# Kernel optimization log

Hardware: AMD Instinct MI355X
Metric: run time of the kernel (lower is better)

The kernel has to match this reference:

```python
import jax, jax.numpy as jnp
import numpy as np

B, L, D = 4, 2048, 1024
H, DK, DV = 16, 64, 64
SCALE = float((4 * DK) ** 0.5)
EPS = 1e-6


def setup_inputs() -> dict:
    key = jax.random.key(0)
    ks = jax.random.split(key, 16)
    s_in = 1.0 / np.sqrt(D)
    inp = {}
    for i, name in enumerate(["q_a", "k_a", "v_a", "q_s", "k_s", "v_s"]):
        inp[name] = jax.random.normal(ks[i], (B, L, D), dtype=jnp.float32)
    # weights stored as [in, out] so projection is x @ W (equivalent math to nn.Linear)
    for j, name in enumerate(["Wqa", "Wka", "Wva", "Wqs", "Wks", "Wvs", "Wfc"]):
        inp[name] = jax.random.normal(ks[6 + j], (D, D), dtype=jnp.float32) * s_in
    inp["gamma"] = jnp.ones((D,), dtype=jnp.float32)
    inp["beta"] = jnp.zeros((D,), dtype=jnp.float32)
    return inp


def _proj(x, W, dh):
    # [B,L,D] @ [D, H*dh] -> [B,H,L,dh]
    return (x @ W).reshape(B, -1, H, dh).transpose(0, 2, 1, 3)


def reference(q_a, k_a, v_a, q_s, k_s, v_s, Wqa, Wka, Wva, Wqs, Wks, Wvs, Wfc, gamma, beta):
    residual = q_a + q_s
    qa = _proj(q_a, Wqa, DK)
    ka = _proj(k_a, Wka, DK)
    va = _proj(v_a, Wva, DV)
    qs = _proj(q_s, Wqs, DK)
    ks_ = _proj(k_s, Wks, DK)
    vs = _proj(v_s, Wvs, DV)
    # a2a + a2s + s2a + s2s == (qa+qs) @ (ka+ks)^T  (algebraic identity)
    q = qa + qs
    k = ka + ks_
    v = va + vs
    scores = jnp.einsum("bhqd,bhkd->bhqk", q, k) / SCALE
    attn = jax.nn.softmax(scores, axis=-1)  # dropout = identity (eval)
    out = jnp.einsum("bhqk,bhkd->bhqd", attn, v)  # [B,H,L,DV]
    out = out.transpose(0, 2, 1, 3).reshape(B, L, H * DV)
    out = out @ Wfc + residual
    mu = jnp.mean(out, axis=-1, keepdims=True)
    var = jnp.var(out, axis=-1, keepdims=True)
    out = (out - mu) * jax.lax.rsqrt(var + EPS) * gamma + beta
    return out
```

## Files before the change

kernel.cpp:

```cpp
#include <hip/hip_runtime.h>
#include <hip/hip_bf16.h>
#include <stdint.h>

typedef __attribute__((ext_vector_type(4))) float f32x4;
typedef __attribute__((ext_vector_type(16))) float f32x16;
typedef __attribute__((ext_vector_type(8))) short short8;
typedef __attribute__((ext_vector_type(2))) int int2v;

#define DEV static __device__ __forceinline__

DEV unsigned short f2bf(float f) {
  unsigned u = __float_as_uint(f);
  u += 0x7fffu + ((u >> 16) & 1u);
  return (unsigned short)(u >> 16);
}

DEV uint32_t cvtpk(float a, float b) {
  uint32_t r;
  asm("v_cvt_pk_bf16_f32 %0, %1, %2" : "=v"(r) : "v"(a), "v"(b));
  return r;
}

DEV int2v pl32(int a, int b) {
  return __builtin_amdgcn_permlane32_swap(a, b, false, false);
}

typedef const __attribute__((address_space(1))) void* gas_ptr;
typedef __attribute__((address_space(3))) void* las_ptr;

DEV void gload_lds16(const void* g, void* l) {
  __builtin_amdgcn_global_load_lds((gas_ptr)g, (las_ptr)l, 16, 0, 0);
}

struct CvtArgs {
  const float* in[6];
  unsigned short* out[6];
};

__global__ __launch_bounds__(256) void cvt_kernel(CvtArgs a, int n4) {
  const float* __restrict__ in = a.in[blockIdx.y];
  unsigned short* __restrict__ out = a.out[blockIdx.y];
  int idx = blockIdx.x * blockDim.x + threadIdx.x;
  int stride = gridDim.x * blockDim.x;
  for (int i = idx; i < n4; i += stride) {
    float4 v = reinterpret_cast<const float4*>(in)[i];
    ushort4 o;
    o.x = f2bf(v.x); o.y = f2bf(v.y); o.z = f2bf(v.z); o.w = f2bf(v.w);
    reinterpret_cast<ushort4*>(out)[i] = o;
  }
}

struct TcvtArgs {
  const float* src[7];
  unsigned short* dst[7];
  int stride[7];
  int koff[7];
};

__global__ __launch_bounds__(256) void tcvt_kernel(TcvtArgs a) {
  const int which = blockIdx.z;
  const float* __restrict__ src = a.src[which];
  unsigned short* __restrict__ dst = a.dst[which];
  const int dstStride = a.stride[which], kOff = a.koff[which];
  __shared__ float tile[32][33];
  int tx = threadIdx.x & 31;
  int ty = threadIdx.x >> 5;
  int n0 = blockIdx.x * 32;
  int k0 = blockIdx.y * 32;
#pragma unroll
  for (int i = 0; i < 4; i++)
    tile[ty + 8 * i][tx] = src[(size_t)(k0 + ty + 8 * i) * 1024 + n0 + tx];
  __syncthreads();
#pragma unroll
  for (int i = 0; i < 4; i++) {
    int n = n0 + ty + 8 * i;
    dst[(size_t)n * dstStride + kOff + k0 + tx] = f2bf(tile[tx][ty + 8 * i]);
  }
}

struct G3Args {
  const unsigned short* A1[3];
  const unsigned short* A2[3];
  const unsigned short* WT[3];
  unsigned short* out[3];
};

__global__ __launch_bounds__(512, 2) void gemm3_kernel(G3Args g) {
  __shared__ unsigned short As[2][256 * 64];
  __shared__ unsigned short Bs[2][256 * 64];
  const int orig = blockIdx.x;
  const int swz = (orig & 7) * 48 + (orig >> 3);
  const int which = swz >> 7;
  const int bid = swz & 127;
  const unsigned short* __restrict__ A1 = g.A1[which];
  const unsigned short* __restrict__ A2 = g.A2[which];
  const unsigned short* __restrict__ WT = g.WT[which];
  unsigned short* __restrict__ outp = g.out[which];

  const int tid = threadIdx.x;
  const int lane = tid & 63;
  const int w = tid >> 6;
  const int mt = bid >> 2, nt = bid & 3;
  const int m0 = mt * 256, n0 = nt * 256;
  const int wr = w >> 2, wc = w & 3;

  const int lr = lane >> 3;
  const int lcsw = (((lane & 7) ^ lr) << 3);
  const int aW = (w < 4) ? (w * 8) : (128 + (w - 4) * 8);
  const int bW = w * 8;

  const int la = lane & 15;
  const int szb = (lane & 7) << 4;
  int cF[2];
#pragma unroll
  for (int ks = 0; ks < 2; ks++)
    cF[ks] = (((ks << 6) + ((lane >> 4) << 4)) ^ szb) >> 1;
  const int arA = (wr * 128 + la) * 64;
  const int brB = (wc * 64 + la) * 64;

  f32x4 zero4 = {0.f, 0.f, 0.f, 0.f};
  f32x4 acc[8][4];
#pragma unroll
  for (int mf = 0; mf < 8; mf++)
#pragma unroll
    for (int nf = 0; nf < 4; nf++) acc[mf][nf] = zero4;

  short8 bf[4][2];

  auto STAGE_B = [&](int buf, int kk) {
#pragma unroll
    for (int r = 0; r < 4; r++)
      gload_lds16(WT + (size_t)(n0 + bW + r * 64 + lr) * 2048 + kk + lcsw,
                  &Bs[buf][(bW + r * 64) * 64 + lane * 8]);
  };
  auto STAGE_A = [&](int buf, int kk, int r) {
    const unsigned short* Ab = (kk < 1024) ? A1 : A2;
    const int ka = kk & 1023;
    gload_lds16(Ab + (size_t)(m0 + aW + r * 32 + lr) * 1024 + ka + lcsw,
                &As[buf][(aW + r * 32) * 64 + lane * 8]);
  };

  STAGE_B(0, 0);
#pragma unroll
  for (int r = 0; r < 4; r++) STAGE_A(0, 0, r);
  asm volatile("s_waitcnt vmcnt(3)" ::: "memory");
  __builtin_amdgcn_s_barrier();
  __builtin_amdgcn_sched_barrier(0);

  for (int kt = 0; kt < 32; kt++) {
    const int cur = kt & 1;
    const int nbuf = cur ^ 1;
    const int kk = kt << 6;
    const int nk = (kt < 31) ? (kk + 64) : kk;
#pragma unroll
    for (int p = 0; p < 4; p++) {
      if (p == 0) {
#pragma unroll
        for (int nf = 0; nf < 4; nf++)
#pragma unroll
          for (int ks = 0; ks < 2; ks++)
            bf[nf][ks] = *reinterpret_cast<const short8*>(&Bs[cur][brB + nf * 1024 + cF[ks]]);
      }
      short8 af[2][2];
#pragma unroll
      for (int mi = 0; mi < 2; mi++)
#pragma unroll
        for (int ks = 0; ks < 2; ks++)
          af[mi][ks] =
              *reinterpret_cast<const short8*>(&As[cur][arA + (2 * p + mi) * 1024 + cF[ks]]);
      if (p == 0) STAGE_B(nbuf, nk);
      STAGE_A(nbuf, nk, p);
      asm volatile("s_waitcnt lgkmcnt(0)" ::: "memory");
      __builtin_amdgcn_sched_barrier(0);
      __builtin_amdgcn_s_setprio(1);
#pragma unroll
      for (int mi = 0; mi < 2; mi++)
#pragma unroll
        for (int nf = 0; nf < 4; nf++)
#pragma unroll
          for (int ks = 0; ks < 2; ks++)
            acc[2 * p + mi][nf] = __builtin_amdgcn_mfma_f32_16x16x32_bf16(
                af[mi][ks], bf[nf][ks], acc[2 * p + mi][nf], 0, 0, 0);
      __builtin_amdgcn_s_setprio(0);
      __builtin_amdgcn_sched_barrier(0);
      if (p == 3) asm volatile("s_waitcnt vmcnt(3)" ::: "memory");
      else        asm volatile("s_waitcnt vmcnt(7)" ::: "memory");
      __builtin_amdgcn_s_barrier();
      __builtin_amdgcn_sched_barrier(0);
    }
  }
  asm volatile("s_waitcnt vmcnt(0)" ::: "memory");

#pragma unroll
  for (int mf = 0; mf < 8; mf++) {
#pragma unroll
    for (int nf = 0; nf < 4; nf++) {
      const int col = n0 + wc * 64 + nf * 16 + (lane & 15);
      const int rbase = m0 + wr * 128 + mf * 16 + ((lane >> 4) << 2);
      const int h = col >> 6, d = col & 63;
      if (which < 2) {
#pragma unroll
        for (int r = 0; r < 4; r++) {
          const int m = rbase + r;
          const int b = m >> 11, l = m & 2047;
          outp[((size_t)((b * 16 + h) * 2048 + l)) * 64 + d] = f2bf(acc[mf][nf][r]);
        }
      } else {
        const int m = rbase;
        const int b = m >> 11, l = m & 2047;
        const int bh = b * 16 + h;
        ushort4 o;
        o.x = f2bf(acc[mf][nf][0]);
        o.y = f2bf(acc[mf][nf][1]);
        o.z = f2bf(acc[mf][nf][2]);
        o.w = f2bf(acc[mf][nf][3]);
        *reinterpret_cast<ushort4*>(
            outp + (size_t)(bh * 64 + (l >> 5)) * 2048 + d * 32 + (l & 31)) = o;
      }
    }
  }
}

__global__ __launch_bounds__(256) void gemmfc_kernel(const unsigned short* __restrict__ A1,
                                                     const unsigned short* __restrict__ WT,
                                                     float* __restrict__ outp) {
  __shared__ unsigned short As[128 * 32];
  __shared__ unsigned short Bs[128 * 32];
  const int orig = blockIdx.x;
  const int bid = (orig & 7) * 64 + (orig >> 3);
  const int tid = threadIdx.x;
  const int lane = tid & 63;
  const int w = tid >> 6;
  const int mt = bid >> 3, nt = bid & 7;
  const int m0 = mt * 128, n0 = nt * 128;

  const int srow = (w << 4) + (lane >> 2);
  const int scol = (lane & 3) << 3;

  f32x4 zero4 = {0.f, 0.f, 0.f, 0.f};
  f32x4 acc[4][4];
#pragma unroll
  for (int mi = 0; mi < 4; mi++)
#pragma unroll
    for (int ni = 0; ni < 4; ni++) acc[mi][ni] = zero4;

  const int wr = w >> 1, wc = w & 1;
  const int arow = (wr << 6) + (lane & 15);
  const int brow = (wc << 6) + (lane & 15);
  const int kcol = (lane >> 4) << 3;

  for (int kt = 0; kt < 32; kt++) {
    const int kk = kt << 5;
#pragma unroll
    for (int p = 0; p < 2; p++) {
      const unsigned short* gp = A1 + (size_t)(m0 + p * 64 + srow) * 1024 + kk + scol;
      gload_lds16(gp, &As[(p * 64 + srow) * 32 + scol]);
    }
#pragma unroll
    for (int p = 0; p < 2; p++) {
      const unsigned short* gp = WT + (size_t)(n0 + p * 64 + srow) * 1024 + kk + scol;
      gload_lds16(gp, &Bs[(p * 64 + srow) * 32 + scol]);
    }
    __syncthreads();

    short8 av[4], bv[4];
#pragma unroll
    for (int mi = 0; mi < 4; mi++)
      av[mi] = *reinterpret_cast<const short8*>(&As[(arow + mi * 16) * 32 + kcol]);
#pragma unroll
    for (int ni = 0; ni < 4; ni++)
      bv[ni] = *reinterpret_cast<const short8*>(&Bs[(brow + ni * 16) * 32 + kcol]);
#pragma unroll
    for (int mi = 0; mi < 4; mi++)
#pragma unroll
      for (int ni = 0; ni < 4; ni++)
        acc[mi][ni] = __builtin_amdgcn_mfma_f32_16x16x32_bf16(av[mi], bv[ni], acc[mi][ni], 0, 0, 0);
    __syncthreads();
  }

#pragma unroll
  for (int mi = 0; mi < 4; mi++) {
#pragma unroll
    for (int ni = 0; ni < 4; ni++) {
      const int col = n0 + (wc << 6) + ni * 16 + (lane & 15);
      const int rbase = m0 + (wr << 6) + mi * 16 + ((lane >> 4) << 2);
#pragma unroll
      for (int r = 0; r < 4; r++)
        outp[(size_t)(rbase + r) * 1024 + col] = acc[mi][ni][r];
    }
  }
}

__global__ __launch_bounds__(256) void attn_kernel(const unsigned short* __restrict__ Q,
                                                   const unsigned short* __restrict__ K,
                                                   const unsigned short* __restrict__ Vt,
                                                   unsigned short* __restrict__ O) {
  __shared__ unsigned short Ks[2][2048];
  __shared__ unsigned short Vs[2][2048];
  const int tid = threadIdx.x;
  const int lane = tid & 63;
  const int w = tid >> 6;
  const int n = blockIdx.x;
  const int bh = (n & 7) * 8 + (n >> 7);
  const int qg = (n >> 3) & 15;
  const int q0 = qg * 128 + w * 32;
  const int lo = lane & 31, hi = lane >> 5;

  const unsigned short* qp = Q + ((size_t)bh * 2048 + q0 + lo) * 64 + (hi << 3);
  short8 qf[4];
#pragma unroll
  for (int c = 0; c < 4; c++)
    qf[c] = *reinterpret_cast<const short8*>(qp + c * 16);

  f32x16 o0 = {0.f,0.f,0.f,0.f,0.f,0.f,0.f,0.f,0.f,0.f,0.f,0.f,0.f,0.f,0.f,0.f};
  f32x16 o1 = {0.f,0.f,0.f,0.f,0.f,0.f,0.f,0.f,0.f,0.f,0.f,0.f,0.f,0.f,0.f,0.f};
  float mrun = -1e30f, lsum = 0.0f;
  const float KS = 1.44269504088896f / 16.0f;

  const char* Kg = (const char*)(K + (size_t)bh * 2048 * 64);
  const char* Vg = (const char*)(Vt + (size_t)bh * 131072);

  const int p16 = tid * 16;
  const int lswz = p16 ^ (((p16 >> 7) & 7) << 4);
  const int koff = lswz;
  const int voff = (lswz >> 7) * 64 + ((lswz >> 6) & 1) * 2048 + (lswz & 63);

  const int sK = (lo & 7) << 4;
  int kix[4];
#pragma unroll
  for (int c = 0; c < 4; c++)
    kix[c] = ((lo * 128 + hi * 16 + c * 32) ^ sK) >> 1;
  int vix[4];
  vix[0] = ((lo * 128 + hi * 16) ^ sK) >> 1;
  vix[1] = ((lo * 128 + 32 + hi * 16) ^ sK) >> 1;
  vix[2] = ((lo * 128 + 64 + hi * 16) ^ sK) >> 1;
  vix[3] = ((lo * 128 + 96 + hi * 16) ^ sK) >> 1;

  auto STAGE = [&](int kt, int buf) {
    gload_lds16(Kg + (size_t)kt * 4096 + koff, &Ks[buf][tid * 8]);
    gload_lds16(Vg + (size_t)kt * 4096 + voff, &Vs[buf][tid * 8]);
  };

  STAGE(0, 0);
  __syncthreads();

  for (int kt = 0; kt < 64; kt++) {
    const int buf = kt & 1;
    const int nx = (kt < 63) ? kt + 1 : 63;
    STAGE(nx, buf ^ 1);

    short8 kc[4], vc[4];
#pragma unroll
    for (int c = 0; c < 4; c++)
      kc[c] = *reinterpret_cast<const short8*>(&Ks[buf][kix[c]]);
#pragma unroll
    for (int c = 0; c < 4; c++)
      vc[c] = *reinterpret_cast<const short8*>(&Vs[buf][vix[c]]);

    f32x16 s = {0.f,0.f,0.f,0.f,0.f,0.f,0.f,0.f,0.f,0.f,0.f,0.f,0.f,0.f,0.f,0.f};
    __builtin_amdgcn_s_setprio(1);
#pragma unroll
    for (int c = 0; c < 4; c++)
      s = __builtin_amdgcn_mfma_f32_32x32x16_bf16(kc[c], qf[c], s, 0, 0, 0);
    __builtin_amdgcn_s_setprio(0);

    float m01 = fmaxf(s[0], s[1]), m23 = fmaxf(s[2], s[3]);
    float m45 = fmaxf(s[4], s[5]), m67 = fmaxf(s[6], s[7]);
    float m89 = fmaxf(s[8], s[9]), mab = fmaxf(s[10], s[11]);
    float mcd = fmaxf(s[12], s[13]), mef = fmaxf(s[14], s[15]);
    float cmax = fmaxf(fmaxf(fmaxf(m01, m23), fmaxf(m45, m67)),
                       fmaxf(fmaxf(m89, mab), fmaxf(mcd, mef)));
    {
      int2v mm = pl32(__float_as_int(cmax), __float_as_int(cmax));
      cmax = fmaxf(__int_as_float(mm.x), __int_as_float(mm.y));
    }

    if (__any(cmax > mrun + 128.0f)) {
      const float mnew = fmaxf(mrun, cmax);
      const float alpha = __builtin_amdgcn_exp2f((mrun - mnew) * KS);
      lsum *= alpha;
#pragma unroll
      for (int r = 0; r < 16; r++) {
        const int row = (r & 3) + ((r >> 2) << 3) + (hi << 2);
        const float ar = __shfl(alpha, row);
        o0[r] *= ar;
        o1[r] *= ar;
      }
      mrun = mnew;
    }

    float pr[16];
    const float mk = mrun * KS;
#pragma unroll
    for (int r = 0; r < 16; r++)
      pr[r] = __builtin_amdgcn_exp2f(__builtin_fmaf(s[r], KS, -mk));
    float c01 = (pr[0] + pr[1]) + (pr[2] + pr[3]);
    float c23 = (pr[4] + pr[5]) + (pr[6] + pr[7]);
    float c45 = (pr[8] + pr[9]) + (pr[10] + pr[11]);
    float c67 = (pr[12] + pr[13]) + (pr[14] + pr[15]);
    float csum = (c01 + c23) + (c45 + c67);
    {
      int2v ss = pl32(__float_as_int(csum), __float_as_int(csum));
      csum = __int_as_float(ss.x) + __int_as_float(ss.y);
    }
    lsum += csum;

    const uint32_t c0 = cvtpk(pr[0], pr[1]),   c1 = cvtpk(pr[2], pr[3]);
    const uint32_t c2 = cvtpk(pr[4], pr[5]),   c3 = cvtpk(pr[6], pr[7]);
    const uint32_t c4 = cvtpk(pr[8], pr[9]),   c5 = cvtpk(pr[10], pr[11]);
    const uint32_t c6 = cvtpk(pr[12], pr[13]), c7 = cvtpk(pr[14], pr[15]);
    int2v s02 = pl32((int)c0, (int)c2);
    int2v s13 = pl32((int)c1, (int)c3);
    int2v s46 = pl32((int)c4, (int)c6);
    int2v s57 = pl32((int)c5, (int)c7);
    union { uint32_t u[4]; short8 v; } pa, pb;
    pa.u[0] = (uint32_t)s02.x; pa.u[1] = (uint32_t)s13.x;
    pa.u[2] = (uint32_t)s02.y; pa.u[3] = (uint32_t)s13.y;
    pb.u[0] = (uint32_t)s46.x; pb.u[1] = (uint32_t)s57.x;
    pb.u[2] = (uint32_t)s46.y; pb.u[3] = (uint32_t)s57.y;

    __builtin_amdgcn_s_setprio(1);
    o0 = __builtin_amdgcn_mfma_f32_32x32x16_bf16(pa.v, vc[0], o0, 0, 0, 0);
    o0 = __builtin_amdgcn_mfma_f32_32x32x16_bf16(pb.v, vc[1], o0, 0, 0, 0);
    o1 = __builtin_amdgcn_mfma_f32_32x32x16_bf16(pa.v, vc[2], o1, 0, 0, 0);
    o1 = __builtin_amdgcn_mfma_f32_32x32x16_bf16(pb.v, vc[3], o1, 0, 0, 0);
    __builtin_amdgcn_s_setprio(0);

    __syncthreads();
  }

  const int b = bh >> 4, h = bh & 15;
#pragma unroll
  for (int r = 0; r < 16; r++) {
    const int row = (r & 3) + ((r >> 2) << 3) + (hi << 2);
    const float lr = __shfl(lsum, row);
    const float inv = __builtin_amdgcn_rcpf(lr);
    const size_t base = ((size_t)b * 2048 + q0 + row) * 1024 + h * 64 + lo;
    O[base] = f2bf(o0[r] * inv);
    O[base + 32] = f2bf(o1[r] * inv);
  }
}

__global__ __launch_bounds__(256) void ln_kernel(const float* __restrict__ fc,
                                                 const float* __restrict__ qa,
                                                 const float* __restrict__ qs,
                                                 const float* __restrict__ gamma,
                                                 const float* __restrict__ beta,
                                                 float* __restrict__ out) {
  const int m = blockIdx.x;
  const int t = threadIdx.x;
  const size_t base = (size_t)m * 1024 + t * 4;
  float4 x = *reinterpret_cast<const float4*>(fc + base);
  const float4 a = *reinterpret_cast<const float4*>(qa + base);
  const float4 b = *reinterpret_cast<const float4*>(qs + base);
  x.x += a.x + b.x; x.y += a.y + b.y; x.z += a.z + b.z; x.w += a.w + b.w;
  float s1 = x.x + x.y + x.z + x.w;
  float s2 = x.x * x.x + x.y * x.y + x.z * x.z + x.w * x.w;
#pragma unroll
  for (int off = 1; off < 64; off <<= 1) {
    s1 += __shfl_xor(s1, off);
    s2 += __shfl_xor(s2, off);
  }
  __shared__ float sh[8];
  const int w = t >> 6, lane = t & 63;
  if (lane == 0) { sh[w] = s1; sh[4 + w] = s2; }
  __syncthreads();
  s1 = sh[0] + sh[1] + sh[2] + sh[3];
  s2 = sh[4] + sh[5] + sh[6] + sh[7];
  const float mu = s1 * (1.0f / 1024.0f);
  const float var = s2 * (1.0f / 1024.0f) - mu * mu;
  const float rs = rsqrtf(var + 1e-6f);
  const float4 g = *reinterpret_cast<const float4*>(gamma + t * 4);
  const float4 be = *reinterpret_cast<const float4*>(beta + t * 4);
  float4 y;
  y.x = (x.x - mu) * rs * g.x + be.x;
  y.y = (x.y - mu) * rs * g.y + be.y;
  y.z = (x.z - mu) * rs * g.z + be.z;
  y.w = (x.w - mu) * rs * g.w + be.w;
  *reinterpret_cast<float4*>(out + base) = y;
}

__global__ void sentinel_kernel(float* out, int n) {
  int i = blockIdx.x * blockDim.x + threadIdx.x;
  if (i < n) out[i] = 1234.5f;
}

extern "C" void kernel_launch(void* const* d_in, const int* in_sizes, int n_in,
                              void* d_out, int out_size, void* d_ws, size_t ws_size,
                              hipStream_t stream) {
  const size_t MB = 1024ull * 1024ull;
  if (ws_size < 174 * MB) {
    sentinel_kernel<<<(out_size + 255) / 256, 256, 0, stream>>>((float*)d_out, out_size);
    return;
  }
  const float* fin[6];
  for (int i = 0; i < 6; i++) fin[i] = (const float*)d_in[i];
  const float* Wf[7];
  for (int i = 0; i < 7; i++) Wf[i] = (const float*)d_in[6 + i];
  const float* gamma = (const float*)d_in[13];
  const float* beta = (const float*)d_in[14];

  char* ws = (char*)d_ws;
  unsigned short* Abf[6];
  for (int i = 0; i < 6; i++) Abf[i] = (unsigned short*)(ws + (size_t)i * 16 * MB);
  unsigned short* WqT = (unsigned short*)(ws + 96 * MB);
  unsigned short* WkT = (unsigned short*)(ws + 100 * MB);
  unsigned short* WvT = (unsigned short*)(ws + 104 * MB);
  unsigned short* WfcT = (unsigned short*)(ws + 108 * MB);
  unsigned short* Qb = (unsigned short*)(ws + 110 * MB);
  unsigned short* Kb = (unsigned short*)(ws + 126 * MB);
  unsigned short* Vtb = (unsigned short*)(ws + 142 * MB);
  unsigned short* Ob = (unsigned short*)(ws + 158 * MB);
  float* fcout = (float*)(ws + 16 * MB);

  CvtArgs ca;
  for (int i = 0; i < 6; i++) { ca.in[i] = fin[i]; ca.out[i] = Abf[i]; }
  cvt_kernel<<<dim3(1024, 6), 256, 0, stream>>>(ca, 2097152);

  TcvtArgs ta;
  const int wsel[7] = {0, 3, 1, 4, 2, 5, 6};
  unsigned short* wdst[7] = {WqT, WqT, WkT, WkT, WvT, WvT, WfcT};
  for (int i = 0; i < 7; i++) {
    ta.src[i] = Wf[wsel[i]];
    ta.dst[i] = wdst[i];
    ta.stride[i] = (i < 6) ? 2048 : 1024;
    ta.koff[i] = (i < 6) ? ((i & 1) ? 1024 : 0) : 0;
  }
  tcvt_kernel<<<dim3(32, 32, 7), 256, 0, stream>>>(ta);

  G3Args g3;
  g3.A1[0] = Abf[0]; g3.A2[0] = Abf[3]; g3.WT[0] = WqT; g3.out[0] = Qb;
  g3.A1[1] = Abf[1]; g3.A2[1] = Abf[4]; g3.WT[1] = WkT; g3.out[1] = Kb;
  g3.A1[2] = Abf[2]; g3.A2[2] = Abf[5]; g3.WT[2] = WvT; g3.out[2] = Vtb;
  gemm3_kernel<<<384, 512, 0, stream>>>(g3);

  attn_kernel<<<1024, 256, 0, stream>>>(Qb, Kb, Vtb, Ob);

  gemmfc_kernel<<<512, 256, 0, stream>>>(Ob, WfcT, fcout);

  ln_kernel<<<8192, 256, 0, stream>>>(fcout, fin[0], fin[3], gamma, beta, (float*)d_out);
}
```

Baseline: 372.5 us.

## Deepen projection GEMM global-to-LDS prefetch to two K-tiles ahead

Restructures the projection GEMM main loop so global-to-LDS loads are issued two K-tiles ahead instead of one. B and A tile loads are spread across the four MFMA phases, with the current buffer refilled for k+2 once its B fragments are in registers. A peeled epilogue drains the last two tiles. The aim is to hide global memory latency better, at the cost of more outstanding loads, hand-tuned vmcnt thresholds that must be exact, and more code.

```diff
diff --git a/kernel.cpp b/kernel.cpp
--- a/kernel.cpp
+++ b/kernel.cpp
@@ -127,11 +127,9 @@
 
   short8 bf[4][2];
 
-  auto STAGE_B = [&](int buf, int kk) {
-#pragma unroll
-    for (int r = 0; r < 4; r++)
-      gload_lds16(WT + (size_t)(n0 + bW + r * 64 + lr) * 2048 + kk + lcsw,
-                  &Bs[buf][(bW + r * 64) * 64 + lane * 8]);
+  auto STAGE_B1 = [&](int buf, int kk, int r) {
+    gload_lds16(WT + (size_t)(n0 + bW + r * 64 + lr) * 2048 + kk + lcsw,
+                &Bs[buf][(bW + r * 64) * 64 + lane * 8]);
   };
   auto STAGE_A = [&](int buf, int kk, int r) {
     const unsigned short* Ab = (kk < 1024) ? A1 : A2;
@@ -139,57 +137,138 @@
     gload_lds16(Ab + (size_t)(m0 + aW + r * 32 + lr) * 1024 + ka + lcsw,
                 &As[buf][(aW + r * 32) * 64 + lane * 8]);
   };
-
-  STAGE_B(0, 0);
-#pragma unroll
-  for (int r = 0; r < 4; r++) STAGE_A(0, 0, r);
-  asm volatile("s_waitcnt vmcnt(3)" ::: "memory");
+  auto READ_B = [&](int buf) {
+#pragma unroll
+    for (int nf = 0; nf < 4; nf++)
+#pragma unroll
+      for (int ks = 0; ks < 2; ks++)
+        bf[nf][ks] = *reinterpret_cast<const short8*>(&Bs[buf][brB + nf * 1024 + cF[ks]]);
+  };
+
+#define READ_A(buf, p, af)                                                               \
+  _Pragma("unroll") for (int mi = 0; mi < 2; mi++)                                       \
+      _Pragma("unroll") for (int ks = 0; ks < 2; ks++)                                   \
+          af[mi][ks] = *reinterpret_cast<const short8*>(                                 \
+              &As[buf][arA + (2 * (p) + mi) * 1024 + cF[ks]]);
+
+#define MFMA_P(p, af)                                                                    \
+  _Pragma("unroll") for (int mi = 0; mi < 2; mi++)                                       \
+      _Pragma("unroll") for (int nf = 0; nf < 4; nf++)                                   \
+          _Pragma("unroll") for (int ks = 0; ks < 2; ks++)                               \
+              acc[2 * (p) + mi][nf] = __builtin_amdgcn_mfma_f32_16x16x32_bf16(           \
+                  af[mi][ks], bf[nf][ks], acc[2 * (p) + mi][nf], 0, 0, 0);
+
+  STAGE_B1(0, 0, 0); STAGE_B1(0, 0, 1); STAGE_A(0, 0, 0);
+  STAGE_B1(0, 0, 2); STAGE_B1(0, 0, 3); STAGE_A(0, 0, 1);
+  STAGE_A(0, 0, 2);
+  STAGE_A(0, 0, 3);
+  STAGE_B1(1, 64, 0); STAGE_B1(1, 64, 1); STAGE_A(1, 64, 0);
+  STAGE_B1(1, 64, 2); STAGE_B1(1, 64, 3); STAGE_A(1, 64, 1);
+  STAGE_A(1, 64, 2);
+  asm volatile("s_waitcnt vmcnt(9)" ::: "memory");
   __builtin_amdgcn_s_barrier();
   __builtin_amdgcn_sched_barrier(0);
 
-  for (int kt = 0; kt < 32; kt++) {
+  for (int kt = 0; kt < 30; kt++) {
     const int cur = kt & 1;
-    const int nbuf = cur ^ 1;
-    const int kk = kt << 6;
-    const int nk = (kt < 31) ? (kk + 64) : kk;
-#pragma unroll
-    for (int p = 0; p < 4; p++) {
-      if (p == 0) {
-#pragma unroll
-        for (int nf = 0; nf < 4; nf++)
-#pragma unroll
-          for (int ks = 0; ks < 2; ks++)
-            bf[nf][ks] = *reinterpret_cast<const short8*>(&Bs[cur][brB + nf * 1024 + cF[ks]]);
-      }
+    const int nxt = cur ^ 1;
+    const int kk1 = (kt + 1) << 6;
+    const int kk2 = (kt + 2) << 6;
+    {
+      READ_B(cur);
       short8 af[2][2];
-#pragma unroll
-      for (int mi = 0; mi < 2; mi++)
-#pragma unroll
-        for (int ks = 0; ks < 2; ks++)
-          af[mi][ks] =
-              *reinterpret_cast<const short8*>(&As[cur][arA + (2 * p + mi) * 1024 + cF[ks]]);
-      if (p == 0) STAGE_B(nbuf, nk);
-      STAGE_A(nbuf, nk, p);
+      READ_A(cur, 0, af);
+      STAGE_A(nxt, kk1, 3);
       asm volatile("s_waitcnt lgkmcnt(0)" ::: "memory");
       __builtin_amdgcn_sched_barrier(0);
       __builtin_amdgcn_s_setprio(1);
-#pragma unroll
-      for (int mi = 0; mi < 2; mi++)
-#pragma unroll
-        for (int nf = 0; nf < 4; nf++)
-#pragma unroll
-          for (int ks = 0; ks < 2; ks++)
-            acc[2 * p + mi][nf] = __builtin_amdgcn_mfma_f32_16x16x32_bf16(
-                af[mi][ks], bf[nf][ks], acc[2 * p + mi][nf], 0, 0, 0);
+      MFMA_P(0, af);
       __builtin_amdgcn_s_setprio(0);
       __builtin_amdgcn_sched_barrier(0);
-      if (p == 3) asm volatile("s_waitcnt vmcnt(3)" ::: "memory");
-      else        asm volatile("s_waitcnt vmcnt(7)" ::: "memory");
       __builtin_amdgcn_s_barrier();
       __builtin_amdgcn_sched_barrier(0);
     }
-  }
-  asm volatile("s_waitcnt vmcnt(0)" ::: "memory");
+    {
+      short8 af[2][2];
+      READ_A(cur, 1, af);
+      STAGE_B1(cur, kk2, 0); STAGE_B1(cur, kk2, 1); STAGE_A(cur, kk2, 0);
+      asm volatile("s_waitcnt lgkmcnt(0)" ::: "memory");
+      __builtin_amdgcn_sched_barrier(0);
+      __builtin_amdgcn_s_setprio(1);
+      MFMA_P(1, af);
+      __builtin_amdgcn_s_setprio(0);
+      __builtin_amdgcn_sched_barrier(0);
+      asm volatile("s_waitcnt vmcnt(12)" ::: "memory");
+      __builtin_amdgcn_s_barrier();
+      __builtin_amdgcn_sched_barrier(0);
+    }
+    {
+      short8 af[2][2];
+      READ_A(cur, 2, af);
+      STAGE_B1(cur, kk2, 2); STAGE_B1(cur, kk2, 3); STAGE_A(cur, kk2, 1);
+      asm volatile("s_waitcnt lgkmcnt(0)" ::: "memory");
+      __builtin_amdgcn_sched_barrier(0);
+      __builtin_amdgcn_s_setprio(1);
+      MFMA_P(2, af);
+      __builtin_amdgcn_s_setprio(0);
+      __builtin_amdgcn_sched_barrier(0);
+      asm volatile("s_waitcnt vmcnt(14)" ::: "memory");
+      __builtin_amdgcn_s_barrier();
+      __builtin_amdgcn_sched_barrier(0);
+    }
+    {
+      short8 af[2][2];
+      READ_A(cur, 3, af);
+      STAGE_A(cur, kk2, 2);
+      asm volatile("s_waitcnt lgkmcnt(0)" ::: "memory");
+      __builtin_amdgcn_sched_barrier(0);
+      __builtin_amdgcn_s_setprio(1);
+      MFMA_P(3, af);
+      __builtin_amdgcn_s_setprio(0);
+      __builtin_amdgcn_sched_barrier(0);
+      asm volatile("s_waitcnt vmcnt(9)" ::: "memory");
+      __builtin_amdgcn_s_barrier();
+      __builtin_amdgcn_sched_barrier(0);
+    }
+  }
+
+  {
+    READ_B(0);
+    short8 af[2][2];
+    READ_A(0, 0, af);
+    STAGE_A(1, 1984, 3);
+    asm volatile("s_waitcnt lgkmcnt(0)" ::: "memory");
+    __builtin_amdgcn_sched_barrier(0);
+    __builtin_amdgcn_s_setprio(1);
+    MFMA_P(0, af);
+    __builtin_amdgcn_s_setprio(0);
+    __builtin_amdgcn_sched_barrier(0);
+    asm volatile("s_waitcnt vmcnt(0)" ::: "memory");
+    __builtin_amdgcn_s_barrier();
+    __builtin_amdgcn_sched_barrier(0);
+#pragma unroll
+    for (int p = 1; p < 4; p++) {
+      short8 af2[2][2];
+      READ_A(0, p, af2);
+      asm volatile("s_waitcnt lgkmcnt(0)" ::: "memory");
+      __builtin_amdgcn_sched_barrier(0);
+      MFMA_P(p, af2);
+    }
+    READ_B(1);
+    short8 af3[2][2];
+    READ_A(1, 0, af3);
+    asm volatile("s_waitcnt lgkmcnt(0)" ::: "memory");
+    __builtin_amdgcn_sched_barrier(0);
+    MFMA_P(0, af3);
+#pragma unroll
+    for (int p = 1; p < 4; p++) {
+      short8 af4[2][2];
+      READ_A(1, p, af4);
+      asm volatile("s_waitcnt lgkmcnt(0)" ::: "memory");
+      __builtin_amdgcn_sched_barrier(0);
+      MFMA_P(p, af4);
+    }
+  }
 
 #pragma unroll
   for (int mf = 0; mf < 8; mf++) {
```

Measured after the change: 376.2 us. Within noise of the previous version (+1.0%).
